# Optimization experiments

Measured on AMD Instinct MI355X. Metric: run time of the kernel, lower is better.

The kernel has to match this reference:

```python
import jax, jax.numpy as jnp
import numpy as np
from functools import partial

NUM_ITERS = 3
NUM_CAPS = 8      # primary capsule count
NUM_CLASSES = 10
OUT_CH = 16       # digit capsule dim
INPUT_SIZE = 32 * 6 * 6  # 1152 primary capsule units per capsule map


def squash(s, axis=-1):
    # faithful to non_linear_squashing: s * (||s||^2/(1+||s||^2)) / (||s||+1e-10)
    norm_sqr = jnp.sum(s * s, axis=axis, keepdims=True)
    scale = jnp.sqrt(norm_sqr) + 1e-10
    mag = norm_sqr / (1.0 + norm_sqr)
    return s * mag / scale


def conv2d(x, w, b, stride):
    y = jax.lax.conv_general_dilated(
        x, w, window_strides=(stride, stride), padding='VALID',
        dimension_numbers=('NCHW', 'OIHW', 'NCHW'))
    return y + b[None, :, None, None]


def setup_inputs() -> dict:
    key = jax.random.key(0)
    ks = jax.random.split(key, 6)
    B = 256
    x = jax.random.normal(ks[0], (B, 1, 28, 28), dtype=jnp.float32)
    conv_w = jax.random.normal(ks[1], (256, 1, 9, 9), dtype=jnp.float32) * 0.05
    conv_b = jax.random.normal(ks[2], (256,), dtype=jnp.float32) * 0.05
    # 8 primary capsule conv units (256->32 each) fused into one 256->256 conv
    prim_w = jax.random.normal(ks[3], (NUM_CAPS * 32, 256, 9, 9), dtype=jnp.float32) * 0.02
    prim_b = jax.random.normal(ks[4], (NUM_CAPS * 32,), dtype=jnp.float32) * 0.02
    # digit routing weights (input_size, num_classes, out_channels, num_capsules)
    digit_w = jax.random.normal(ks[5], (INPUT_SIZE, NUM_CLASSES, OUT_CH, NUM_CAPS), dtype=jnp.float32)
    return {'x': x, 'conv_w': conv_w, 'conv_b': conv_b,
            'prim_w': prim_w, 'prim_b': prim_b, 'digit_w': digit_w}


def reference(x, conv_w, conv_b, prim_w, prim_b, digit_w):
    B = x.shape[0]
    # conv stack: 1->256 k9 s1 + ReLU  (28 -> 20); pool is MaxPool2d(1,1) = identity
    h = jax.nn.relu(conv2d(x, conv_w, conv_b, stride=1))  # (B,256,20,20)
    # primary capsules: 8 convs 256->32 k9 s2, no activation (nl_activation=False)
    p = conv2d(h, prim_w, prim_b, stride=2)               # (B,256,6,6)
    u = p.reshape(B, NUM_CAPS, -1)                        # (B,8,1152)
    u = squash(u, axis=-1)
    # digit layer with dynamic routing
    # u_i: (B, IS, 8);  u_j_i[b,i,c,o] = sum_k W[i,c,o,k] * u_i[b,i,k]
    u_i = jnp.transpose(u, (0, 2, 1))                     # (B,1152,8)
    u_j_i = jnp.einsum('icok,bik->bico', digit_w, u_i)    # (B,1152,10,16)
    b_ij = jnp.zeros((INPUT_SIZE, NUM_CLASSES), dtype=x.dtype)
    out = None
    for _ in range(NUM_ITERS):
        c_ij = jax.nn.softmax(b_ij, axis=0)               # softmax over input capsules (dim=1 in torch)
        s_j = jnp.einsum('ic,bico->bco', c_ij, u_j_i)     # (B,10,16)
        # original squashes (B,1,C,16,1) along dim=2 == the CLASS axis
        out = squash(s_j, axis=1)                         # (B,10,16)
        # agreement: mean over batch of <u_j_i, v_j>
        u_v = jnp.einsum('bico,bco->ic', u_j_i, out) / B  # (1152,10)
        b_ij = b_ij + u_v
    # torch returns out.squeeze(1) with shape (B, C, 16, 1)
    return out[..., None]
```

## Files before the change

### kernel.cpp

```cpp
#include <hip/hip_runtime.h>
#include <cstdint>
#include <cstddef>


typedef __attribute__((ext_vector_type(8))) short short8;
typedef __attribute__((ext_vector_type(4))) float f32x4;

#define PHALF 2359296

__device__ __forceinline__ unsigned short f2bf_rn(float x) {
    unsigned u = __float_as_uint(x);
    unsigned r = (u + 0x7fffu + ((u >> 16) & 1u)) >> 16;
    return (unsigned short)r;
}

__global__ void k_makew(const float* __restrict__ w2,
                        unsigned short* __restrict__ wt) {
    __shared__ float lw[20736];
    int ocg = blockIdx.x, icg = blockIdx.y, t = threadIdx.x;
    for (int idx = t; idx < 20736; idx += 256) {
        int row = idx / 81, k = idx % 81;
        int oc_l = row >> 5, ic_l = row & 31;
        lw[idx] = w2[((size_t)(ocg * 8 + oc_l) * 256 + icg * 32 + ic_l) * 81 + k];
    }
    __syncthreads();
    for (int idx = t; idx < 2592; idx += 256) {
        int k = idx >> 5;
        int r = idx & 31;
        int oc_l = r >> 2, sl = r & 3;
        unsigned short hi8[8];
        #pragma unroll
        for (int j = 0; j < 8; j++)
            hi8[j] = f2bf_rn(lw[(oc_l * 32 + sl * 8 + j) * 81 + k]);
        size_t o = ((size_t)(k * 256 + ocg * 8 + oc_l)) * 256 + icg * 32 + sl * 8;
        *(uint4*)&wt[o] = *(uint4*)hi8;
    }
}

__global__ void k_conv1(const float* __restrict__ x, const float* __restrict__ cw,
                        const float* __restrict__ cb,
                        unsigned short* __restrict__ h) {
    __shared__ float img[784];
    __shared__ float wsm[32 * 81];
    int b = blockIdx.x, ocg = blockIdx.y, t = threadIdx.x;
    for (int idx = t; idx < 784; idx += 256) img[idx] = x[b * 784 + idx];
    for (int idx = t; idx < 2592; idx += 256) wsm[idx] = cw[ocg * 2592 + idx];
    __syncthreads();
    int oc_l = t & 31, g = t >> 5;
    int oc = ocg * 32 + oc_l;
    float bias = cb[oc];
    const float* wp = &wsm[oc_l * 81];
    for (int q = g; q < 100; q += 8) {
        int py = q / 5, qx = (q % 5) * 4;
        float a0 = bias, a1 = bias, a2 = bias, a3 = bias;
        #pragma unroll
        for (int ky = 0; ky < 9; ky++) {
            const float* ir = &img[(py + ky) * 28 + qx];
            float r[12];
            #pragma unroll
            for (int j = 0; j < 12; j++) r[j] = ir[j];
            #pragma unroll
            for (int kx = 0; kx < 9; kx++) {
                float w = wp[ky * 9 + kx];
                a0 += r[kx] * w; a1 += r[kx + 1] * w;
                a2 += r[kx + 2] * w; a3 += r[kx + 3] * w;
            }
        }
        float v[4] = { fmaxf(a0, 0.f), fmaxf(a1, 0.f), fmaxf(a2, 0.f), fmaxf(a3, 0.f) };
        size_t base = ((size_t)b * 400 + py * 20 + qx) * 256 + oc;
        #pragma unroll
        for (int j = 0; j < 4; j++)
            h[base + (size_t)j * 256] = f2bf_rn(v[j]);
    }
}

__global__ __launch_bounds__(256) void k_conv2m(
    const unsigned short* __restrict__ h,
    const unsigned short* __restrict__ wt,
    float* __restrict__ pp)
{
    __shared__ unsigned short smem[24576];
    const int t = threadIdx.x;
    const int w = t >> 6, l = t & 63;
    const int mb = blockIdx.x, nb = blockIdx.y, z = blockIdx.z;

    const unsigned short* src;
    int nld, sbase;
    unsigned rowbase[16];
    if (w < 2) {
        src = h; nld = 16; sbase = w * 8192;
        #pragma unroll
        for (int ld = 0; ld < 16; ld++) {
            int row = ld * 8 + (l >> 3);
            int c = l & 7;
            int g = c ^ (row & 7);
            int P = mb * 128 + row;
            int b = P / 36, o = P % 36;
            int oy = o / 6, ox = o % 6;
            rowbase[ld] = (unsigned)((b * 400 + oy * 40 + ox * 2) * 256 + z * 128 + w * 64 + g * 8);
        }
    } else {
        int hh = w - 2;
        src = wt; nld = 8; sbase = 16384 + hh * 4096;
        #pragma unroll
        for (int ld = 0; ld < 8; ld++) {
            int oc = ld * 8 + (l >> 3);
            int c = l & 7;
            int g = c ^ (oc & 7);
            rowbase[ld] = (unsigned)((nb * 64 + oc) * 256 + z * 128 + hh * 64 + g * 8);
        }
    }

    const int wm = w & 1, wn = w >> 1;
    const int lane16 = l & 15, q = l >> 4;

    f32x4 acc[4][2] = {};

    for (int ky = 0; ky < 9; ky++) {
        for (int kx = 0; kx < 9; kx++) {
            const unsigned kofs = (w < 2) ? (unsigned)((ky * 20 + kx) * 256)
                                          : (unsigned)((ky * 9 + kx) * 65536);
            __syncthreads();
            for (int ld = 0; ld < nld; ld++) {
                __builtin_amdgcn_global_load_lds(
                    (const __attribute__((address_space(1))) unsigned int*)(const void*)(src + rowbase[ld] + kofs),
                    (__attribute__((address_space(3))) unsigned int*)(void*)(smem + sbase + ld * 512),
                    16, 0, 0);
            }
            __syncthreads();
            #pragma unroll
            for (int hh = 0; hh < 2; hh++) {
                #pragma unroll
                for (int ic2 = 0; ic2 < 2; ic2++) {
                    short8 a[4], b[2];
                    #pragma unroll
                    for (int mt = 0; mt < 4; mt++) {
                        int pixL = wm * 64 + mt * 16 + lane16;
                        int ps = (ic2 * 4 + q) ^ (pixL & 7);
                        a[mt] = *(const short8*)(smem + hh * 8192 + pixL * 64 + ps * 8);
                    }
                    #pragma unroll
                    for (int nt = 0; nt < 2; nt++) {
                        int ocL = wn * 32 + nt * 16 + lane16;
                        int ps = (ic2 * 4 + q) ^ (ocL & 7);
                        b[nt] = *(const short8*)(smem + 16384 + hh * 4096 + ocL * 64 + ps * 8);
                    }
                    #pragma unroll
                    for (int mt = 0; mt < 4; mt++)
                        #pragma unroll
                        for (int nt = 0; nt < 2; nt++)
                            acc[mt][nt] = __builtin_amdgcn_mfma_f32_16x16x32_bf16(a[mt], b[nt], acc[mt][nt], 0, 0, 0);
                }
            }
        }
    }

    float* pout = pp + (size_t)z * PHALF;
    #pragma unroll
    for (int mt = 0; mt < 4; mt++) {
        int pixG = mb * 128 + wm * 64 + mt * 16 + q * 4;
        int b = pixG / 36, p36 = pixG % 36;
        #pragma unroll
        for (int nt = 0; nt < 2; nt++) {
            int oc = nb * 64 + wn * 32 + nt * 16 + lane16;
            f32x4 v = acc[mt][nt];
            *(f32x4*)&pp[0] ;
            *(f32x4*)&pout[((size_t)(b * 256 + oc)) * 36 + p36] = v;
        }
    }
}

__global__ void k_squash1(const float* __restrict__ pp, const float* __restrict__ prim_b,
                          float* __restrict__ U) {
    __shared__ float red[4];
    int b = blockIdx.x >> 3, cap = blockIdx.x & 7;
    int t = threadIdx.x;
    const float* pa = pp + ((size_t)b * 256 + cap * 32) * 36;
    const float* pc = pa + PHALF;
    float v[5];
    float ss = 0.f;
    #pragma unroll
    for (int j = 0; j < 5; j++) {
        int idx = t + j * 256;
        if (idx < 1152) {
            int ch_l = idx / 36;
            float val = pa[idx] + pc[idx] + prim_b[cap * 32 + ch_l];
            v[j] = val; ss += val * val;
        } else v[j] = 0.f;
    }
    for (int off = 32; off; off >>= 1) ss += __shfl_down(ss, off);
    if ((t & 63) == 0) red[t >> 6] = ss;
    __syncthreads();
    float n2 = red[0] + red[1] + red[2] + red[3];
    float f = (n2 / (1.0f + n2)) / (sqrtf(n2) + 1e-10f);
    #pragma unroll
    for (int j = 0; j < 5; j++) {
        int idx = t + j * 256;
        if (idx < 1152) U[(size_t)b * 9216 + idx * 8 + cap] = v[j] * f;
    }
}

__global__ void k_dwt2(const float* __restrict__ dw, float* __restrict__ dwT2) {
    int co = blockIdx.x, t = threadIdx.x;
    int c = co >> 4, o = co & 15;
    const float* base = dw + c * 128 + o * 8;
    float* out = dwT2 + (size_t)co * 9216;
    for (int idx = t; idx < 9216; idx += 256) {
        int i = idx >> 3, k = idx & 7;
        out[idx] = base[(size_t)i * 1280 + k];
    }
}

__global__ void k_ut(const float* __restrict__ U, float* __restrict__ UT) {
    __shared__ float tl[64][65];
    int ikb = blockIdx.x, bb = blockIdx.y, t = threadIdx.x;
    for (int idx = t; idx < 1024; idx += 256) {
        int row = idx >> 4, c4 = idx & 15;
        float4 v = *(const float4*)&U[(size_t)(bb * 64 + row) * 9216 + ikb * 64 + c4 * 4];
        tl[c4 * 4 + 0][row] = v.x;
        tl[c4 * 4 + 1][row] = v.y;
        tl[c4 * 4 + 2][row] = v.z;
        tl[c4 * 4 + 3][row] = v.w;
    }
    __syncthreads();
    for (int idx = t; idx < 1024; idx += 256) {
        int row = idx >> 4, c4 = idx & 15;
        float4 v = make_float4(tl[row][c4 * 4 + 0], tl[row][c4 * 4 + 1],
                               tl[row][c4 * 4 + 2], tl[row][c4 * 4 + 3]);
        *(float4*)&UT[(size_t)(ikb * 64 + row) * 256 + bb * 64 + c4 * 4] = v;
    }
}

__global__ void k_softmax(const float* __restrict__ bij, float* __restrict__ csm) {
    __shared__ float red[4];
    int c = blockIdx.x, t = threadIdx.x;
    float vals[5];
    float mx = -1e30f;
    #pragma unroll
    for (int j = 0; j < 5; j++) {
        int i = t + j * 256;
        vals[j] = (i < 1152) ? bij[i * 10 + c] : -1e30f;
        mx = fmaxf(mx, vals[j]);
    }
    for (int off = 32; off; off >>= 1) mx = fmaxf(mx, __shfl_down(mx, off));
    if ((t & 63) == 0) red[t >> 6] = mx;
    __syncthreads();
    mx = fmaxf(fmaxf(red[0], red[1]), fmaxf(red[2], red[3]));
    __syncthreads();
    float s = 0.f;
    #pragma unroll
    for (int j = 0; j < 5; j++) {
        int i = t + j * 256;
        vals[j] = (i < 1152) ? expf(vals[j] - mx) : 0.f;
        s += vals[j];
    }
    for (int off = 32; off; off >>= 1) s += __shfl_down(s, off);
    if ((t & 63) == 0) red[t >> 6] = s;
    __syncthreads();
    s = red[0] + red[1] + red[2] + red[3];
    float inv = 1.0f / s;
    #pragma unroll
    for (int j = 0; j < 5; j++) {
        int i = t + j * 256;
        if (i < 1152) csm[i * 10 + c] = vals[j] * inv;
    }
}

__global__ __launch_bounds__(256) void k_gemm1(const float* __restrict__ U,
                                               const float* __restrict__ dwT2,
                                               const float* __restrict__ csm,
                                               float* __restrict__ part,
                                               int uniform) {
    __shared__ float Us[32 * 36];
    __shared__ float WsT[5120];
    __shared__ float cl[360];
    int mb = blockIdx.x, kc = blockIdx.y, t = threadIdx.x;
    int tc = t & 15, tb = t >> 4;
    if (!uniform)
        for (int idx = t; idx < 360; idx += 256) cl[idx] = csm[kc * 360 + idx];
    const float uscale = 1.0f / 1152.0f;
    float acc[2][10] = {};
    for (int ks = 0; ks < 9; ks++) {
        __syncthreads();
        {
            int bb = t >> 3, k4 = t & 7;
            *(float4*)&Us[bb * 36 + k4 * 4] =
                *(const float4*)&U[(size_t)(mb * 32 + bb) * 9216 + kc * 288 + ks * 32 + k4 * 4];
        }
        #pragma unroll
        for (int pass = 0; pass < 5; pass++) {
            int s = t + pass * 256;
            int co = s >> 3, p = s & 7;
            int kq = p ^ (co & 7);
            int ikl = ks * 32 + kq * 4;
            float4 v = *(const float4*)&dwT2[(size_t)co * 9216 + kc * 288 + ikl];
            float sc = uniform ? uscale : cl[(ikl >> 3) * 10 + (co >> 4)];
            v.x *= sc; v.y *= sc; v.z *= sc; v.w *= sc;
            *(float4*)&WsT[s * 4] = v;
        }
        __syncthreads();
        float a0[32], a1[32];
        #pragma unroll
        for (int kq = 0; kq < 8; kq++) {
            float4 v0 = *(const float4*)&Us[(tb * 2) * 36 + kq * 4];
            float4 v1 = *(const float4*)&Us[(tb * 2 + 1) * 36 + kq * 4];
            a0[kq * 4 + 0] = v0.x; a0[kq * 4 + 1] = v0.y; a0[kq * 4 + 2] = v0.z; a0[kq * 4 + 3] = v0.w;
            a1[kq * 4 + 0] = v1.x; a1[kq * 4 + 1] = v1.y; a1[kq * 4 + 2] = v1.z; a1[kq * 4 + 3] = v1.w;
        }
        #pragma unroll
        for (int j = 0; j < 10; j++) {
            int co = tc + 16 * j;
            int cx = co & 7, cbase = co * 32;
            #pragma unroll
            for (int kq = 0; kq < 8; kq++) {
                float4 wv = *(const float4*)&WsT[cbase + ((kq ^ cx) << 2)];
                acc[0][j] += a0[kq * 4 + 0] * wv.x; acc[0][j] += a0[kq * 4 + 1] * wv.y;
                acc[0][j] += a0[kq * 4 + 2] * wv.z; acc[0][j] += a0[kq * 4 + 3] * wv.w;
                acc[1][j] += a1[kq * 4 + 0] * wv.x; acc[1][j] += a1[kq * 4 + 1] * wv.y;
                acc[1][j] += a1[kq * 4 + 2] * wv.z; acc[1][j] += a1[kq * 4 + 3] * wv.w;
            }
        }
    }
    #pragma unroll
    for (int r = 0; r < 2; r++)
        #pragma unroll
        for (int j = 0; j < 10; j++)
            part[(size_t)kc * 40960 + (mb * 32 + tb * 2 + r) * 160 + tc + 16 * j] = acc[r][j];
}

__global__ void k_redsq(const float* __restrict__ part, float* __restrict__ out,
                        float* __restrict__ outT, int writeT) {
    __shared__ float sl[160];
    __shared__ float n2s[16];
    int b = blockIdx.x, t = threadIdx.x;
    float s = 0.f;
    if (t < 160) {
        for (int kc = 0; kc < 32; kc++) s += part[(size_t)kc * 40960 + b * 160 + t];
        sl[t] = s;
    }
    __syncthreads();
    if (t < 16) {
        float n2 = 0.f;
        #pragma unroll
        for (int c = 0; c < 10; c++) { float v = sl[c * 16 + t]; n2 += v * v; }
        n2s[t] = n2;
    }
    __syncthreads();
    if (t < 160) {
        float n2 = n2s[t & 15];
        float f = (n2 / (1.0f + n2)) / (sqrtf(n2) + 1e-10f);
        float r = s * f;
        out[(size_t)b * 160 + t] = r;
        if (writeT) outT[(size_t)t * 256 + b] = r;
    }
}

__global__ __launch_bounds__(256) void k_g2uv(const float* __restrict__ UT,
                                              const float* __restrict__ outTg,
                                              const float* __restrict__ dw,
                                              float* __restrict__ bij) {
    __shared__ float UsT[1024];
    __shared__ float OsT[5120];
    __shared__ float dwl[5120];
    __shared__ float sb[320];
    int blk = blockIdx.x, t = threadIdx.x;
    int tc = t & 15, tm = t >> 4;
    for (int idx = t; idx < 5120; idx += 256)
        dwl[idx] = dw[(size_t)blk * 5120 + idx];
    float acc[2][10] = {};
    for (int bs = 0; bs < 256; bs += 32) {
        __syncthreads();
        {
            int m = t >> 3, p = t & 7;
            int kq = p ^ (m & 7);
            *(float4*)&UsT[t * 4] =
                *(const float4*)&UT[(size_t)(blk * 32 + m) * 256 + bs + kq * 4];
        }
        #pragma unroll
        for (int pass = 0; pass < 5; pass++) {
            int s = t + pass * 256;
            int co = s >> 3, p = s & 7;
            int kq = p ^ (co & 7);
            *(float4*)&OsT[s * 4] =
                *(const float4*)&outTg[(size_t)co * 256 + bs + kq * 4];
        }
        __syncthreads();
        float a0[32], a1[32];
        int m0 = tm * 2, m1 = tm * 2 + 1;
        #pragma unroll
        for (int kq = 0; kq < 8; kq++) {
            float4 v0 = *(const float4*)&UsT[m0 * 32 + ((kq ^ (m0 & 7)) << 2)];
            float4 v1 = *(const float4*)&UsT[m1 * 32 + ((kq ^ (m1 & 7)) << 2)];
            a0[kq * 4 + 0] = v0.x; a0[kq * 4 + 1] = v0.y; a0[kq * 4 + 2] = v0.z; a0[kq * 4 + 3] = v0.w;
            a1[kq * 4 + 0] = v1.x; a1[kq * 4 + 1] = v1.y; a1[kq * 4 + 2] = v1.z; a1[kq * 4 + 3] = v1.w;
        }
        #pragma unroll
        for (int j = 0; j < 10; j++) {
            int co = tc + 16 * j;
            int cx = co & 7, cbase = co * 32;
            #pragma unroll
            for (int kq = 0; kq < 8; kq++) {
                float4 wv = *(const float4*)&OsT[cbase + ((kq ^ cx) << 2)];
                acc[0][j] += a0[kq * 4 + 0] * wv.x; acc[0][j] += a0[kq * 4 + 1] * wv.y;
                acc[0][j] += a0[kq * 4 + 2] * wv.z; acc[0][j] += a0[kq * 4 + 3] * wv.w;
                acc[1][j] += a1[kq * 4 + 0] * wv.x; acc[1][j] += a1[kq * 4 + 1] * wv.y;
                acc[1][j] += a1[kq * 4 + 2] * wv.z; acc[1][j] += a1[kq * 4 + 3] * wv.w;
            }
        }
    }
    #pragma unroll
    for (int r = 0; r < 2; r++) {
        int ik_l = tm * 2 + r;
        int i_l = ik_l >> 3, k = ik_l & 7;
        #pragma unroll
        for (int j = 0; j < 10; j++) {
            float v = acc[r][j] * dwl[i_l * 1280 + (j * 16 + tc) * 8 + k];
            v += __shfl_down(v, 8, 16);
            v += __shfl_down(v, 4, 16);
            v += __shfl_down(v, 2, 16);
            v += __shfl_down(v, 1, 16);
            if (tc == 0) sb[ik_l * 10 + j] = v;
        }
    }
    __syncthreads();
    if (t < 40) {
        int i_l = t / 10, c = t % 10;
        float s = 0.f;
        #pragma unroll
        for (int kk = 0; kk < 8; kk++) s += sb[(i_l * 8 + kk) * 10 + c];
        size_t o = (size_t)(blk * 4 + i_l) * 10 + c;
        bij[o] += s * (1.0f / 256.0f);
    }
}

extern "C" void kernel_launch(void* const* d_in, const int* in_sizes, int n_in,
                              void* d_out, int out_size, void* d_ws, size_t ws_size,
                              hipStream_t stream) {
    const float* x      = (const float*)d_in[0];
    const float* conv_w = (const float*)d_in[1];
    const float* conv_b = (const float*)d_in[2];
    const float* prim_w = (const float*)d_in[3];
    const float* prim_b = (const float*)d_in[4];
    const float* dw     = (const float*)d_in[5];

    char* wsb = (char*)d_ws;
    unsigned short* h  = (unsigned short*)(wsb);
    unsigned short* wt = (unsigned short*)(wsb + 52428800);
    float* pp   = (float*)(wsb + 63045632);
    float* U    = (float*)(wsb + 81920000);
    float* dwT2 = (float*)(wsb + 91357184);
    float* part = (float*)(wsb + 97255424);
    float* csm  = (float*)(wsb + 102498304);
    float* bij  = (float*)(wsb + 102544384);
    float* outT = (float*)(wsb + 102590464);
    float* outw = (float*)(wsb + 102754304);
    float* UT   = (float*)(wsb + 102918144);

    k_makew<<<dim3(32, 8), 256, 0, stream>>>(prim_w, wt);
    k_conv1<<<dim3(256, 8), 256, 0, stream>>>(x, conv_w, conv_b, h);
    k_dwt2<<<160, 256, 0, stream>>>(dw, dwT2);
    k_conv2m<<<dim3(72, 4, 2), 256, 0, stream>>>(h, wt, pp);
    k_squash1<<<2048, 256, 0, stream>>>(pp, prim_b, U);
    k_ut<<<dim3(144, 4), 256, 0, stream>>>(U, UT);
    hipMemsetAsync(bij, 0, 11520 * sizeof(float), stream);

    k_gemm1<<<dim3(8, 32), 256, 0, stream>>>(U, dwT2, csm, part, 1);
    k_redsq<<<256, 256, 0, stream>>>(part, outw, outT, 1);
    k_g2uv<<<288, 256, 0, stream>>>(UT, outT, dw, bij);
    k_softmax<<<10, 256, 0, stream>>>(bij, csm);
    k_gemm1<<<dim3(8, 32), 256, 0, stream>>>(U, dwT2, csm, part, 0);
    k_redsq<<<256, 256, 0, stream>>>(part, outw, outT, 1);
    k_g2uv<<<288, 256, 0, stream>>>(UT, outT, dw, bij);
    k_softmax<<<10, 256, 0, stream>>>(bij, csm);
    k_gemm1<<<dim3(8, 32), 256, 0, stream>>>(U, dwT2, csm, part, 0);
    k_redsq<<<256, 256, 0, stream>>>(part, (float*)d_out, outT, 0);
}
```

Before: 508.0 us.

## Move conv1 to bf16 MFMA, split conv2 K four ways, fuse prep and transpose

The scalar fp32 first convolution becomes a bf16 MFMA im2col kernel, with its weights pre-packed into fragment layout by a new prep kernel. That prep kernel also absorbs the digit-weight transpose and the routing-logit zeroing. The primary conv's split-K grows from 2 to 4 slices with half the shared memory per block, which raises parallelism and occupancy. The squash kernel now sums the four partial slices and writes the transposed UT directly, removing the separate transpose kernel. In exchange, conv1 now rounds its inputs to bf16 and squash reads more partial-sum traffic.

```diff
diff --git a/kernel.cpp b/kernel.cpp
--- a/kernel.cpp
+++ b/kernel.cpp
@@ -37,40 +37,95 @@
     }
 }
 
-__global__ void k_conv1(const float* __restrict__ x, const float* __restrict__ cw,
-                        const float* __restrict__ cb,
-                        unsigned short* __restrict__ h) {
-    __shared__ float img[784];
-    __shared__ float wsm[32 * 81];
-    int b = blockIdx.x, ocg = blockIdx.y, t = threadIdx.x;
-    for (int idx = t; idx < 784; idx += 256) img[idx] = x[b * 784 + idx];
-    for (int idx = t; idx < 2592; idx += 256) wsm[idx] = cw[ocg * 2592 + idx];
-    __syncthreads();
-    int oc_l = t & 31, g = t >> 5;
-    int oc = ocg * 32 + oc_l;
-    float bias = cb[oc];
-    const float* wp = &wsm[oc_l * 81];
-    for (int q = g; q < 100; q += 8) {
-        int py = q / 5, qx = (q % 5) * 4;
-        float a0 = bias, a1 = bias, a2 = bias, a3 = bias;
-        #pragma unroll
-        for (int ky = 0; ky < 9; ky++) {
-            const float* ir = &img[(py + ky) * 28 + qx];
-            float r[12];
+__global__ void k_prep2(const float* __restrict__ cw, const float* __restrict__ dw,
+                        unsigned short* __restrict__ wb1, float* __restrict__ dwT2,
+                        float* __restrict__ bij) {
+    int blk = blockIdx.x, t = threadIdx.x;
+    if (blk == 0) {
+        for (int idx = t; idx < 24576; idx += 256) {
+            int j = idx & 7, lane = (idx >> 3) & 63;
+            int q = (idx >> 9) % 3, nt = idx / 1536;
+            int oc = nt * 16 + (lane & 15);
+            int kg = q * 32 + (lane >> 4) * 8 + j;
+            float v = (kg < 81) ? cw[oc * 81 + kg] : 0.f;
+            wb1[idx] = f2bf_rn(v);
+        }
+    } else if (blk == 1) {
+        for (int idx = t; idx < 11520; idx += 256) bij[idx] = 0.f;
+    } else {
+        int co = blk - 2;
+        int c = co >> 4, o = co & 15;
+        const float* base = dw + c * 128 + o * 8;
+        float* out = dwT2 + (size_t)co * 9216;
+        for (int idx = t; idx < 9216; idx += 256) {
+            int i = idx >> 3, k = idx & 7;
+            out[idx] = base[(size_t)i * 1280 + k];
+        }
+    }
+}
+
+__global__ __launch_bounds__(256) void k_conv1m(
+    const float* __restrict__ x, const unsigned short* __restrict__ wb1,
+    const float* __restrict__ cb, unsigned short* __restrict__ h)
+{
+    __shared__ unsigned short xb[900];
+    int b = blockIdx.x, ng = blockIdx.y, t = threadIdx.x;
+    int w = t >> 6, l = t & 63;
+    for (int idx = t; idx < 900; idx += 256) {
+        int row = idx / 30, col = idx % 30;
+        float v = (row < 28 && col < 28) ? x[(size_t)b * 784 + row * 28 + col] : 0.f;
+        xb[idx] = f2bf_rn(v);
+    }
+    __syncthreads();
+    int lane16 = l & 15, l4 = l >> 4;
+    int ntile = (w == 0) ? 7 : 6;
+    short8 afr[7][3];
+    for (int i = 0; i < 7; i++) {
+        if (i < ntile) {
+            int mt = w + 4 * i;
+            int pix = mt * 16 + lane16;
+            int py = pix / 20, px = pix % 20;
             #pragma unroll
-            for (int j = 0; j < 12; j++) r[j] = ir[j];
-            #pragma unroll
-            for (int kx = 0; kx < 9; kx++) {
-                float w = wp[ky * 9 + kx];
-                a0 += r[kx] * w; a1 += r[kx + 1] * w;
-                a2 += r[kx + 2] * w; a3 += r[kx + 3] * w;
-            }
-        }
-        float v[4] = { fmaxf(a0, 0.f), fmaxf(a1, 0.f), fmaxf(a2, 0.f), fmaxf(a3, 0.f) };
-        size_t base = ((size_t)b * 400 + py * 20 + qx) * 256 + oc;
-        #pragma unroll
-        for (int j = 0; j < 4; j++)
-            h[base + (size_t)j * 256] = f2bf_rn(v[j]);
+            for (int qq = 0; qq < 3; qq++) {
+                int kbase = qq * 32 + l4 * 8;
+                unsigned short tmp[8];
+                int ky = kbase / 9, kx = kbase - 9 * (kbase / 9);
+                #pragma unroll
+                for (int j = 0; j < 8; j++) {
+                    tmp[j] = xb[(py + ky) * 30 + px + kx];
+                    kx++; if (kx == 9) { kx = 0; ky++; }
+                }
+                afr[i][qq] = *(short8*)tmp;
+            }
+        }
+    }
+    for (int nt0 = 0; nt0 < 8; nt0++) {
+        int nt = ng * 8 + nt0;
+        short8 bfr[3];
+        #pragma unroll
+        for (int qq = 0; qq < 3; qq++)
+            bfr[qq] = *(const short8*)&wb1[(nt * 3 + qq) * 512 + l * 8];
+        float bias = cb[nt * 16 + lane16];
+        f32x4 acc[7] = {};
+        for (int i = 0; i < 7; i++) {
+            if (i < ntile) {
+                #pragma unroll
+                for (int qq = 0; qq < 3; qq++)
+                    acc[i] = __builtin_amdgcn_mfma_f32_16x16x32_bf16(afr[i][qq], bfr[qq], acc[i], 0, 0, 0);
+            }
+        }
+        for (int i = 0; i < 7; i++) {
+            if (i < ntile) {
+                int mt = w + 4 * i;
+                int pixb = mt * 16 + l4 * 4;
+                size_t base = ((size_t)b * 400 + pixb) * 256 + nt * 16 + lane16;
+                #pragma unroll
+                for (int r = 0; r < 4; r++) {
+                    float v = fmaxf(acc[i][r] + bias, 0.f);
+                    h[base + (size_t)r * 256] = f2bf_rn(v);
+                }
+            }
+        }
     }
 }
 
@@ -79,35 +134,35 @@
     const unsigned short* __restrict__ wt,
     float* __restrict__ pp)
 {
-    __shared__ unsigned short smem[24576];
+    __shared__ unsigned short smem[12288];
     const int t = threadIdx.x;
     const int w = t >> 6, l = t & 63;
     const int mb = blockIdx.x, nb = blockIdx.y, z = blockIdx.z;
 
     const unsigned short* src;
     int nld, sbase;
-    unsigned rowbase[16];
+    unsigned rowbase[8];
     if (w < 2) {
-        src = h; nld = 16; sbase = w * 8192;
-        #pragma unroll
-        for (int ld = 0; ld < 16; ld++) {
-            int row = ld * 8 + (l >> 3);
+        src = h; nld = 8; sbase = w * 4096;
+        #pragma unroll
+        for (int ld = 0; ld < 8; ld++) {
+            int row = w * 64 + ld * 8 + (l >> 3);
             int c = l & 7;
             int g = c ^ (row & 7);
             int P = mb * 128 + row;
             int b = P / 36, o = P % 36;
             int oy = o / 6, ox = o % 6;
-            rowbase[ld] = (unsigned)((b * 400 + oy * 40 + ox * 2) * 256 + z * 128 + w * 64 + g * 8);
+            rowbase[ld] = (unsigned)((b * 400 + oy * 40 + ox * 2) * 256 + z * 64 + g * 8);
         }
     } else {
         int hh = w - 2;
-        src = wt; nld = 8; sbase = 16384 + hh * 4096;
-        #pragma unroll
-        for (int ld = 0; ld < 8; ld++) {
-            int oc = ld * 8 + (l >> 3);
+        src = wt; nld = 4; sbase = 8192 + hh * 2048;
+        #pragma unroll
+        for (int ld = 0; ld < 4; ld++) {
+            int oc = hh * 32 + ld * 8 + (l >> 3);
             int c = l & 7;
             int g = c ^ (oc & 7);
-            rowbase[ld] = (unsigned)((nb * 64 + oc) * 256 + z * 128 + hh * 64 + g * 8);
+            rowbase[ld] = (unsigned)((nb * 64 + oc) * 256 + z * 64 + g * 8);
         }
     }
 
@@ -129,28 +184,25 @@
             }
             __syncthreads();
             #pragma unroll
-            for (int hh = 0; hh < 2; hh++) {
+            for (int ic2 = 0; ic2 < 2; ic2++) {
+                short8 a[4], b[2];
                 #pragma unroll
-                for (int ic2 = 0; ic2 < 2; ic2++) {
-                    short8 a[4], b[2];
+                for (int mt = 0; mt < 4; mt++) {
+                    int pixL = wm * 64 + mt * 16 + lane16;
+                    int ps = (ic2 * 4 + q) ^ (pixL & 7);
+                    a[mt] = *(const short8*)(smem + pixL * 64 + ps * 8);
+                }
+                #pragma unroll
+                for (int nt = 0; nt < 2; nt++) {
+                    int ocL = wn * 32 + nt * 16 + lane16;
+                    int ps = (ic2 * 4 + q) ^ (ocL & 7);
+                    b[nt] = *(const short8*)(smem + 8192 + ocL * 64 + ps * 8);
+                }
+                #pragma unroll
+                for (int mt = 0; mt < 4; mt++)
                     #pragma unroll
-                    for (int mt = 0; mt < 4; mt++) {
-                        int pixL = wm * 64 + mt * 16 + lane16;
-                        int ps = (ic2 * 4 + q) ^ (pixL & 7);
-                        a[mt] = *(const short8*)(smem + hh * 8192 + pixL * 64 + ps * 8);
-                    }
-                    #pragma unroll
-                    for (int nt = 0; nt < 2; nt++) {
-                        int ocL = wn * 32 + nt * 16 + lane16;
-                        int ps = (ic2 * 4 + q) ^ (ocL & 7);
-                        b[nt] = *(const short8*)(smem + 16384 + hh * 4096 + ocL * 64 + ps * 8);
-                    }
-                    #pragma unroll
-                    for (int mt = 0; mt < 4; mt++)
-                        #pragma unroll
-                        for (int nt = 0; nt < 2; nt++)
-                            acc[mt][nt] = __builtin_amdgcn_mfma_f32_16x16x32_bf16(a[mt], b[nt], acc[mt][nt], 0, 0, 0);
-                }
+                    for (int nt = 0; nt < 2; nt++)
+                        acc[mt][nt] = __builtin_amdgcn_mfma_f32_16x16x32_bf16(a[mt], b[nt], acc[mt][nt], 0, 0, 0);
             }
         }
     }
@@ -164,19 +216,17 @@
         for (int nt = 0; nt < 2; nt++) {
             int oc = nb * 64 + wn * 32 + nt * 16 + lane16;
             f32x4 v = acc[mt][nt];
-            *(f32x4*)&pp[0] ;
             *(f32x4*)&pout[((size_t)(b * 256 + oc)) * 36 + p36] = v;
         }
     }
 }
 
 __global__ void k_squash1(const float* __restrict__ pp, const float* __restrict__ prim_b,
-                          float* __restrict__ U) {
+                          float* __restrict__ U, float* __restrict__ UT) {
     __shared__ float red[4];
     int b = blockIdx.x >> 3, cap = blockIdx.x & 7;
     int t = threadIdx.x;
     const float* pa = pp + ((size_t)b * 256 + cap * 32) * 36;
-    const float* pc = pa + PHALF;
     float v[5];
     float ss = 0.f;
     #pragma unroll
@@ -184,7 +234,8 @@
         int idx = t + j * 256;
         if (idx < 1152) {
             int ch_l = idx / 36;
-            float val = pa[idx] + pc[idx] + prim_b[cap * 32 + ch_l];
+            float val = pa[idx] + pa[idx + PHALF] + pa[idx + 2 * PHALF] +
+                        pa[idx + 3 * PHALF] + prim_b[cap * 32 + ch_l];
             v[j] = val; ss += val * val;
         } else v[j] = 0.f;
     }
@@ -196,38 +247,11 @@
     #pragma unroll
     for (int j = 0; j < 5; j++) {
         int idx = t + j * 256;
-        if (idx < 1152) U[(size_t)b * 9216 + idx * 8 + cap] = v[j] * f;
-    }
-}
-
-__global__ void k_dwt2(const float* __restrict__ dw, float* __restrict__ dwT2) {
-    int co = blockIdx.x, t = threadIdx.x;
-    int c = co >> 4, o = co & 15;
-    const float* base = dw + c * 128 + o * 8;
-    float* out = dwT2 + (size_t)co * 9216;
-    for (int idx = t; idx < 9216; idx += 256) {
-        int i = idx >> 3, k = idx & 7;
-        out[idx] = base[(size_t)i * 1280 + k];
-    }
-}
-
-__global__ void k_ut(const float* __restrict__ U, float* __restrict__ UT) {
-    __shared__ float tl[64][65];
-    int ikb = blockIdx.x, bb = blockIdx.y, t = threadIdx.x;
-    for (int idx = t; idx < 1024; idx += 256) {
-        int row = idx >> 4, c4 = idx & 15;
-        float4 v = *(const float4*)&U[(size_t)(bb * 64 + row) * 9216 + ikb * 64 + c4 * 4];
-        tl[c4 * 4 + 0][row] = v.x;
-        tl[c4 * 4 + 1][row] = v.y;
-        tl[c4 * 4 + 2][row] = v.z;
-        tl[c4 * 4 + 3][row] = v.w;
-    }
-    __syncthreads();
-    for (int idx = t; idx < 1024; idx += 256) {
-        int row = idx >> 4, c4 = idx & 15;
-        float4 v = make_float4(tl[row][c4 * 4 + 0], tl[row][c4 * 4 + 1],
-                               tl[row][c4 * 4 + 2], tl[row][c4 * 4 + 3]);
-        *(float4*)&UT[(size_t)(ikb * 64 + row) * 256 + bb * 64 + c4 * 4] = v;
+        if (idx < 1152) {
+            float r = v[j] * f;
+            U[(size_t)b * 9216 + idx * 8 + cap] = r;
+            UT[(size_t)(idx * 8 + cap) * 256 + b] = r;
+        }
     }
 }
 
@@ -444,25 +468,24 @@
     const float* dw     = (const float*)d_in[5];
 
     char* wsb = (char*)d_ws;
-    unsigned short* h  = (unsigned short*)(wsb);
-    unsigned short* wt = (unsigned short*)(wsb + 52428800);
+    unsigned short* h   = (unsigned short*)(wsb);
+    unsigned short* wt  = (unsigned short*)(wsb + 52428800);
     float* pp   = (float*)(wsb + 63045632);
-    float* U    = (float*)(wsb + 81920000);
-    float* dwT2 = (float*)(wsb + 91357184);
-    float* part = (float*)(wsb + 97255424);
-    float* csm  = (float*)(wsb + 102498304);
-    float* bij  = (float*)(wsb + 102544384);
-    float* outT = (float*)(wsb + 102590464);
-    float* outw = (float*)(wsb + 102754304);
-    float* UT   = (float*)(wsb + 102918144);
+    float* U    = (float*)(wsb + 100794368);
+    float* dwT2 = (float*)(wsb + 110231552);
+    float* part = (float*)(wsb + 116129792);
+    float* csm  = (float*)(wsb + 121372672);
+    float* bij  = (float*)(wsb + 121418752);
+    float* outT = (float*)(wsb + 121464832);
+    float* outw = (float*)(wsb + 121628672);
+    float* UT   = (float*)(wsb + 121792512);
+    unsigned short* wb1 = (unsigned short*)(wsb + 131229696);
 
     k_makew<<<dim3(32, 8), 256, 0, stream>>>(prim_w, wt);
-    k_conv1<<<dim3(256, 8), 256, 0, stream>>>(x, conv_w, conv_b, h);
-    k_dwt2<<<160, 256, 0, stream>>>(dw, dwT2);
-    k_conv2m<<<dim3(72, 4, 2), 256, 0, stream>>>(h, wt, pp);
-    k_squash1<<<2048, 256, 0, stream>>>(pp, prim_b, U);
-    k_ut<<<dim3(144, 4), 256, 0, stream>>>(U, UT);
-    hipMemsetAsync(bij, 0, 11520 * sizeof(float), stream);
+    k_prep2<<<162, 256, 0, stream>>>(conv_w, dw, wb1, dwT2, bij);
+    k_conv1m<<<dim3(256, 2), 256, 0, stream>>>(x, wb1, conv_b, h);
+    k_conv2m<<<dim3(72, 4, 4), 256, 0, stream>>>(h, wt, pp);
+    k_squash1<<<2048, 256, 0, stream>>>(pp, prim_b, U, UT);
 
     k_gemm1<<<dim3(8, 32), 256, 0, stream>>>(U, dwT2, csm, part, 1);
     k_redsq<<<256, 256, 0, stream>>>(part, outw, outT, 1);
```

New measurement: 532.3 us. 1.05x slower.
